# Optimization experiments

Hardware: AMD Instinct MI355X
Metric: run time of the kernel (lower is better)

Reference implementation:

```python
import jax, jax.numpy as jnp
import numpy as np

N_NODES = 20000
N_EDGES = 640000
NODE_IN = 128
EDGE_IN = 64
HID = 128
OUT = 128
LOG2 = float(np.log(2.0))


def ssp(x):
    # DGL ShiftedSoftplus: softplus(x) - log(2)
    return jax.nn.softplus(x) - LOG2


def cfconv(x, e, src, dst,
           nW, nb, eW1, eb1, eW2, eb2, oW, ob):
    hv = x @ nW + nb                                  # [N, HID]
    he = ssp(ssp(e @ eW1 + eb1) @ eW2 + eb2)          # [E, HID]
    msg = hv[src] * he                                # gather + filter
    agg = jax.ops.segment_sum(msg, dst, num_segments=N_NODES)
    return ssp(agg @ oW + ob)


def setup_inputs() -> dict:
    key = jax.random.key(0)
    ks = jax.random.split(key, 20)
    def w(k, shape, fan_in):
        return jax.random.normal(k, shape, dtype=jnp.float32) * (1.0 / np.sqrt(fan_in))
    inp = {
        "node_inputs": jax.random.normal(ks[0], (N_NODES, NODE_IN), dtype=jnp.float32),
        "edge_inputs": jax.random.normal(ks[1], (N_EDGES, EDGE_IN), dtype=jnp.float32),
        "src": jax.random.randint(ks[2], (N_EDGES,), 0, N_NODES, dtype=jnp.int32),
        "dst": jax.random.randint(ks[3], (N_EDGES,), 0, N_NODES, dtype=jnp.int32),
        # conv1 params
        "n1_W": w(ks[4], (NODE_IN, HID), NODE_IN), "n1_b": jnp.zeros((HID,), jnp.float32),
        "e1_W1": w(ks[5], (EDGE_IN, HID), EDGE_IN), "e1_b1": jnp.zeros((HID,), jnp.float32),
        "e1_W2": w(ks[6], (HID, HID), HID), "e1_b2": jnp.zeros((HID,), jnp.float32),
        "o1_W": w(ks[7], (HID, HID), HID), "o1_b": jnp.zeros((HID,), jnp.float32),
        # conv2 params
        "n2_W": w(ks[8], (HID, HID), HID), "n2_b": jnp.zeros((HID,), jnp.float32),
        "e2_W1": w(ks[9], (EDGE_IN, HID), EDGE_IN), "e2_b1": jnp.zeros((HID,), jnp.float32),
        "e2_W2": w(ks[10], (HID, HID), HID), "e2_b2": jnp.zeros((HID,), jnp.float32),
        "o2_W": w(ks[11], (HID, OUT), HID), "o2_b": jnp.zeros((OUT,), jnp.float32),
    }
    return inp


def reference(node_inputs, edge_inputs, src, dst,
              n1_W, n1_b, e1_W1, e1_b1, e1_W2, e1_b2, o1_W, o1_b,
              n2_W, n2_b, e2_W1, e2_b1, e2_W2, e2_b2, o2_W, o2_b):
    h = cfconv(node_inputs, edge_inputs, src, dst,
               n1_W, n1_b, e1_W1, e1_b1, e1_W2, e1_b2, o1_W, o1_b)
    h = jnp.tanh(h)
    # dropout(p) is identity in eval mode
    h = cfconv(h, edge_inputs, src, dst,
               n2_W, n2_b, e2_W1, e2_b1, e2_W2, e2_b2, o2_W, o2_b)
    return jnp.tanh(h)
```

## Files before the change

kernel.cpp:

```cpp
#include <hip/hip_runtime.h>
#include <hip/hip_bf16.h>
#include <math.h>

typedef __bf16 bf16x8 __attribute__((ext_vector_type(8)));
typedef float f32x4 __attribute__((ext_vector_type(4)));

#define LOG2F 0.6931471805599453f
#define PK1 72
#define PK2 136

__device__ __forceinline__ float sspf(float x) {
    float t = __expf(-fabsf(x));
    return fmaxf(x, 0.0f) + __logf(1.0f + t) - LOG2F;
}
__device__ __forceinline__ unsigned short f2bf(float f) {
    union { float f; unsigned u; } v; v.f = f;
    unsigned r = v.u + 0x7FFF + ((v.u >> 16) & 1);
    return (unsigned short)(r >> 16);
}
__device__ __forceinline__ unsigned short f2bf_fast(float f) {
    __bf16 h = (__bf16)f;
    return __builtin_bit_cast(unsigned short, h);
}

template<int ACT>
__global__ void node_gemm(const float* __restrict__ X, const float* __restrict__ W,
                          const float* __restrict__ b, float* __restrict__ Y, int N) {
    __shared__ float xs[2][128];
    const int tid = threadIdx.x;
    const int r = tid >> 7;
    const int c = tid & 127;
    const int row = blockIdx.x * 2 + r;
    if (row < N) xs[r][c] = X[(size_t)row * 128 + c];
    __syncthreads();
    if (row >= N) return;
    float acc = b[c];
#pragma unroll 8
    for (int k = 0; k < 128; ++k)
        acc = fmaf(xs[r][k], W[k * 128 + c], acc);
    if (ACT) acc = tanhf(sspf(acc));
    Y[(size_t)row * 128 + c] = acc;
}

__global__ void convert_wT(const float* __restrict__ W, unsigned short* __restrict__ O,
                           int K, int PK) {
    int idx = blockIdx.x * 256 + threadIdx.x;
    if (idx >= 128 * PK) return;
    int n = idx / PK, k = idx - n * PK;
    O[idx] = (k < K) ? f2bf(W[k * 128 + n]) : (unsigned short)0;
}

__global__ void hist_kernel(const int* __restrict__ dst, int* __restrict__ hist, int E) {
    int i = blockIdx.x * 256 + threadIdx.x;
    if (i < E) atomicAdd(&hist[dst[i]], 1);
}
__global__ void scan_kernel(const int* __restrict__ hist, int* __restrict__ row_ptr,
                            int* __restrict__ cursor, int N) {
    __shared__ int part[1024];
    const int tid = threadIdx.x;
    const int chunk = (N + 1023) / 1024;
    const int lo = min(tid * chunk, N);
    const int hi = min(lo + chunk, N);
    int s = 0;
    for (int i = lo; i < hi; ++i) s += hist[i];
    part[tid] = s;
    __syncthreads();
    if (tid == 0) {
        int run = 0;
        for (int i = 0; i < 1024; ++i) { int t = part[i]; part[i] = run; run += t; }
    }
    __syncthreads();
    int run = part[tid];
    for (int i = lo; i < hi; ++i) { row_ptr[i] = run; cursor[i] = run; run += hist[i]; }
}
__global__ void scatter_kernel(const int* __restrict__ dst, int* __restrict__ cursor,
                               int* __restrict__ perm, int E) {
    int i = blockIdx.x * 256 + threadIdx.x;
    if (i < E) { int p = atomicAdd(&cursor[dst[i]], 1); perm[p] = i; }
}
__global__ void sort_buckets(const int* __restrict__ row_ptr, const int* __restrict__ hist,
                             int* __restrict__ perm, int N) {
    int n = blockIdx.x * 256 + threadIdx.x;
    if (n >= N) return;
    const int lo = row_ptr[n], hi = lo + hist[n];
    for (int i = lo + 1; i < hi; ++i) {
        int v = perm[i]; int j = i - 1;
        while (j >= lo && perm[j] > v) { perm[j + 1] = perm[j]; --j; }
        perm[j + 1] = v;
    }
}
__global__ void permute_sd(const int* __restrict__ perm, const int* __restrict__ src,
                           const int* __restrict__ dst, int* __restrict__ srcP,
                           int* __restrict__ dstP, int E) {
    int i = blockIdx.x * 256 + threadIdx.x;
    if (i < E) { int e = perm[i]; srcP[i] = src[e]; dstP[i] = dst[e]; }
}
__global__ void permute_e(const int* __restrict__ perm, const float* __restrict__ Ef,
                          unsigned short* __restrict__ Ebf, int nE) {
    long long idx = (long long)blockIdx.x * 256 + threadIdx.x;
    if (idx >= (long long)nE * 16) return;
    int p = (int)(idx >> 4), q = (int)(idx & 15);
    int e = perm[p];
    float4 v = *(const float4*)&Ef[(size_t)e * 64 + q * 4];
    unsigned short* o = &Ebf[(size_t)p * 64 + q * 4];
    o[0] = f2bf_fast(v.x); o[1] = f2bf_fast(v.y);
    o[2] = f2bf_fast(v.z); o[3] = f2bf_fast(v.w);
}

template<int MODE>
__global__ __launch_bounds__(256) void edge_mfma(
    const unsigned short* __restrict__ Ebf, const float* __restrict__ Ef,
    const int* __restrict__ perm,
    const int* __restrict__ srcA, const int* __restrict__ dstA,
    const float* __restrict__ HV,
    const unsigned short* __restrict__ W1T, const float* __restrict__ b1,
    const unsigned short* __restrict__ W2T, const float* __restrict__ b2,
    float* __restrict__ AGG, int nE)
{
    __shared__ unsigned short sT1[64 * PK2];
    __shared__ int sSrc[64], sDst[64];
    __shared__ unsigned short sE[(MODE == 1) ? 64 * PK1 : 4];

    const int tid = threadIdx.x;
    const int e0 = blockIdx.x * 64;

    if (tid < 64) {
        int gi = min(e0 + tid, nE - 1);
        sSrc[tid] = srcA[gi];
        sDst[tid] = dstA[gi];
    }
    if (MODE == 1) {
        const int r = tid >> 2, c0 = (tid & 3) * 16;
        int gi = e0 + r;
        int e = (gi < nE) ? (perm ? perm[gi] : gi) : 0;
        const float4* s4 = (const float4*)&Ef[(size_t)e * 64 + c0];
        unsigned short* dr = &sE[r * PK1 + c0];
#pragma unroll
        for (int j = 0; j < 4; ++j) {
            float4 v = s4[j];
            dr[j*4+0] = f2bf_fast(v.x); dr[j*4+1] = f2bf_fast(v.y);
            dr[j*4+2] = f2bf_fast(v.z); dr[j*4+3] = f2bf_fast(v.w);
        }
    }
    __syncthreads();

    const int w = tid >> 6, l = tid & 63, cb = w * 32, lr = l & 15, hi = l >> 4, lk = hi * 8;
    const float bb1[2] = { b1[cb + lr], b1[cb + 16 + lr] };
    const float bb2[2] = { b2[cb + lr], b2[cb + 16 + lr] };

    bf16x8 B1[2][2];
#pragma unroll
    for (int nt = 0; nt < 2; ++nt)
#pragma unroll
        for (int kt = 0; kt < 2; ++kt)
            B1[nt][kt] = *(const bf16x8*)&W1T[(size_t)(cb + nt*16 + lr) * PK1 + kt*32 + lk];

    f32x4 acc1[4][2];
#pragma unroll
    for (int mt = 0; mt < 4; ++mt)
#pragma unroll
        for (int nt = 0; nt < 2; ++nt)
            acc1[mt][nt] = (f32x4){bb1[nt], bb1[nt], bb1[nt], bb1[nt]};
#pragma unroll
    for (int kt = 0; kt < 2; ++kt)
#pragma unroll
        for (int mt = 0; mt < 4; ++mt) {
            bf16x8 A;
            if (MODE == 0) {
                const int row = min(e0 + mt*16 + lr, nE - 1);
                A = *(const bf16x8*)&Ebf[(size_t)row * 64 + kt*32 + lk];
            } else {
                A = *(const bf16x8*)&sE[(mt*16 + lr) * PK1 + kt*32 + lk];
            }
#pragma unroll
            for (int nt = 0; nt < 2; ++nt)
                acc1[mt][nt] = __builtin_amdgcn_mfma_f32_16x16x32_bf16(A, B1[nt][kt], acc1[mt][nt], 0, 0, 0);
        }

#pragma unroll
    for (int mt = 0; mt < 4; ++mt)
#pragma unroll
        for (int nt = 0; nt < 2; ++nt) {
            const int col = cb + nt*16 + lr;
#pragma unroll
            for (int r = 0; r < 4; ++r) {
                const int row = mt*16 + hi*4 + r;
                sT1[row * PK2 + col] = f2bf_fast(sspf(acc1[mt][nt][r]));
            }
        }
    __syncthreads();

    bf16x8 B2[2][4];
#pragma unroll
    for (int nt = 0; nt < 2; ++nt)
#pragma unroll
        for (int kt = 0; kt < 4; ++kt)
            B2[nt][kt] = *(const bf16x8*)&W2T[(size_t)(cb + nt*16 + lr) * PK2 + kt*32 + lk];

    f32x4 acc2[4][2];
#pragma unroll
    for (int mt = 0; mt < 4; ++mt)
#pragma unroll
        for (int nt = 0; nt < 2; ++nt)
            acc2[mt][nt] = (f32x4){bb2[nt], bb2[nt], bb2[nt], bb2[nt]};
#pragma unroll
    for (int kt = 0; kt < 4; ++kt)
#pragma unroll
        for (int mt = 0; mt < 4; ++mt) {
            bf16x8 A = *(const bf16x8*)&sT1[(mt*16 + lr) * PK2 + kt*32 + lk];
#pragma unroll
            for (int nt = 0; nt < 2; ++nt)
                acc2[mt][nt] = __builtin_amdgcn_mfma_f32_16x16x32_bf16(A, B2[nt][kt], acc2[mt][nt], 0, 0, 0);
        }

    const int col0 = cb + lr, col1 = cb + 16 + lr;
    int curd = sDst[hi * 4];
    float s0 = 0.f, s1 = 0.f;
#pragma unroll
    for (int mt = 0; mt < 4; ++mt) {
#pragma unroll
        for (int r = 0; r < 4; ++r) {
            const int row = mt*16 + hi*4 + r;
            const float msk = (e0 + row < nE) ? 1.f : 0.f;
            const float he0 = sspf(acc2[mt][0][r]) * msk;
            const float he1 = sspf(acc2[mt][1][r]) * msk;
            const int s = sSrc[row], d = sDst[row];
            const float m0 = HV[(size_t)s * 128 + col0] * he0;
            const float m1 = HV[(size_t)s * 128 + col1] * he1;
            if (d != curd) {
                atomicAdd(&AGG[(size_t)curd * 128 + col0], s0);
                atomicAdd(&AGG[(size_t)curd * 128 + col1], s1);
                s0 = 0.f; s1 = 0.f; curd = d;
            }
            s0 += m0; s1 += m1;
        }
    }
    atomicAdd(&AGG[(size_t)curd * 128 + col0], s0);
    atomicAdd(&AGG[(size_t)curd * 128 + col1], s1);
}

extern "C" void kernel_launch(void* const* d_in, const int* in_sizes, int n_in,
                              void* d_out, int out_size, void* d_ws, size_t ws_size,
                              hipStream_t stream) {
    const float* x    = (const float*)d_in[0];
    const float* e    = (const float*)d_in[1];
    const int*   src  = (const int*)  d_in[2];
    const int*   dst  = (const int*)  d_in[3];
    const float* n1W  = (const float*)d_in[4];
    const float* n1b  = (const float*)d_in[5];
    const float* e1W1 = (const float*)d_in[6];
    const float* e1b1 = (const float*)d_in[7];
    const float* e1W2 = (const float*)d_in[8];
    const float* e1b2 = (const float*)d_in[9];
    const float* o1W  = (const float*)d_in[10];
    const float* o1b  = (const float*)d_in[11];
    const float* n2W  = (const float*)d_in[12];
    const float* n2b  = (const float*)d_in[13];
    const float* e2W1 = (const float*)d_in[14];
    const float* e2b1 = (const float*)d_in[15];
    const float* e2W2 = (const float*)d_in[16];
    const float* e2b2 = (const float*)d_in[17];
    const float* o2W  = (const float*)d_in[18];
    const float* o2b  = (const float*)d_in[19];

    const int N = in_sizes[0] / 128;
    const int E = in_sizes[2];
    float* out = (float*)d_out;

    char* ws = (char*)d_ws;
    size_t off = 0;
    auto alloc = [&](size_t bytes) -> char* {
        char* p = ws + off;
        off = (off + bytes + 255) & ~(size_t)255;
        return p;
    };
    float* agg = (float*)alloc((size_t)N * 128 * 4);
    float* hv  = (float*)alloc((size_t)N * 128 * 4);
    unsigned short* w_e1w1 = (unsigned short*)alloc(128 * PK1 * 2);
    unsigned short* w_e1w2 = (unsigned short*)alloc(128 * PK2 * 2);
    unsigned short* w_e2w1 = (unsigned short*)alloc(128 * PK1 * 2);
    unsigned short* w_e2w2 = (unsigned short*)alloc(128 * PK2 * 2);
    int* perm    = (int*)alloc((size_t)E * 4);
    int* srcP    = (int*)alloc((size_t)E * 4);
    int* dstP    = (int*)alloc((size_t)E * 4);
    int* hist    = (int*)alloc((size_t)N * 4);
    int* cursor  = (int*)alloc((size_t)N * 4);
    int* row_ptr = (int*)alloc((size_t)N * 4);
    const size_t sort_need = off;
    unsigned short* Ebf = (unsigned short*)alloc((size_t)E * 64 * 2);
    const bool useEbf  = (ws_size >= off);
    const bool useSort = (ws_size >= sort_need);

    float* hbuf = out;

    convert_wT<<<(128*PK1 + 255)/256, 256, 0, stream>>>(e1W1, w_e1w1, 64,  PK1);
    convert_wT<<<(128*PK2 + 255)/256, 256, 0, stream>>>(e1W2, w_e1w2, 128, PK2);
    convert_wT<<<(128*PK1 + 255)/256, 256, 0, stream>>>(e2W1, w_e2w1, 64,  PK1);
    convert_wT<<<(128*PK2 + 255)/256, 256, 0, stream>>>(e2W2, w_e2w2, 128, PK2);

    const int* sA = src;
    const int* dA = dst;
    const int* permArg = nullptr;
    if (useSort) {
        hipMemsetAsync(hist, 0, (size_t)N * 4, stream);
        hist_kernel<<<(E + 255)/256, 256, 0, stream>>>(dst, hist, E);
        scan_kernel<<<1, 1024, 0, stream>>>(hist, row_ptr, cursor, N);
        scatter_kernel<<<(E + 255)/256, 256, 0, stream>>>(dst, cursor, perm, E);
        sort_buckets<<<(N + 255)/256, 256, 0, stream>>>(row_ptr, hist, perm, N);
        permute_sd<<<(E + 255)/256, 256, 0, stream>>>(perm, src, dst, srcP, dstP, E);
        if (useEbf)
            permute_e<<<(int)(((size_t)E * 16 + 255)/256), 256, 0, stream>>>(perm, e, Ebf, E);
        sA = srcP; dA = dstP; permArg = perm;
    }

    const int nodeBlocks = (N + 1) / 2;
    const int edgeBlocks = (E + 63) / 64;
    const size_t nbytes = (size_t)N * 128 * 4;

    node_gemm<0><<<nodeBlocks, 256, 0, stream>>>(x, n1W, n1b, hv, N);
    hipMemsetAsync(agg, 0, nbytes, stream);
    if (useEbf)
        edge_mfma<0><<<edgeBlocks, 256, 0, stream>>>(Ebf, nullptr, nullptr, sA, dA, hv,
                                                     w_e1w1, e1b1, w_e1w2, e1b2, agg, E);
    else
        edge_mfma<1><<<edgeBlocks, 256, 0, stream>>>(nullptr, e, permArg, sA, dA, hv,
                                                     w_e1w1, e1b1, w_e1w2, e1b2, agg, E);
    node_gemm<1><<<nodeBlocks, 256, 0, stream>>>(agg, o1W, o1b, hbuf, N);

    node_gemm<0><<<nodeBlocks, 256, 0, stream>>>(hbuf, n2W, n2b, hv, N);
    hipMemsetAsync(agg, 0, nbytes, stream);
    if (useEbf)
        edge_mfma<0><<<edgeBlocks, 256, 0, stream>>>(Ebf, nullptr, nullptr, sA, dA, hv,
                                                     w_e2w1, e2b1, w_e2w2, e2b2, agg, E);
    else
        edge_mfma<1><<<edgeBlocks, 256, 0, stream>>>(nullptr, e, permArg, sA, dA, hv,
                                                     w_e2w1, e2b1, w_e2w2, e2b2, agg, E);
    node_gemm<1><<<nodeBlocks, 256, 0, stream>>>(agg, o2W, o2b, out, N);
}
```

Baseline: 787.8 us.

## Move node GEMMs to split-bf16 MFMA, fuse mid-layer GEMMs, merge prep kernels

Replaces the scalar FMA node GEMMs with MFMA kernels that split fp32 operands into bf16 hi/lo pairs and run three MFMAs per tile to keep near-fp32 accuracy. The output GEMM of conv1 and the node GEMM of conv2 are fused into one kernel that keeps the intermediate tile in shared memory. The four weight-conversion launches are merged into one, and permute_sd is folded into permute_e. The edge kernel now issues segment atomics once per 16-row tile instead of only at the end, which looks like a correctness adjustment. The cost is three times the MFMA work and extra weight buffers, in exchange for removing the slow scalar node GEMMs and several launches.

```diff
diff --git a/kernel.cpp b/kernel.cpp
--- a/kernel.cpp
+++ b/kernel.cpp
@@ -18,36 +18,51 @@
     unsigned r = v.u + 0x7FFF + ((v.u >> 16) & 1);
     return (unsigned short)(r >> 16);
 }
+__device__ __forceinline__ float bf2f(unsigned short u) {
+    union { unsigned u; float f; } v; v.u = ((unsigned)u) << 16;
+    return v.f;
+}
 __device__ __forceinline__ unsigned short f2bf_fast(float f) {
     __bf16 h = (__bf16)f;
     return __builtin_bit_cast(unsigned short, h);
 }
 
-template<int ACT>
-__global__ void node_gemm(const float* __restrict__ X, const float* __restrict__ W,
-                          const float* __restrict__ b, float* __restrict__ Y, int N) {
-    __shared__ float xs[2][128];
-    const int tid = threadIdx.x;
-    const int r = tid >> 7;
-    const int c = tid & 127;
-    const int row = blockIdx.x * 2 + r;
-    if (row < N) xs[r][c] = X[(size_t)row * 128 + c];
-    __syncthreads();
-    if (row >= N) return;
-    float acc = b[c];
-#pragma unroll 8
-    for (int k = 0; k < 128; ++k)
-        acc = fmaf(xs[r][k], W[k * 128 + c], acc);
-    if (ACT) acc = tanhf(sspf(acc));
-    Y[(size_t)row * 128 + c] = acc;
-}
-
-__global__ void convert_wT(const float* __restrict__ W, unsigned short* __restrict__ O,
-                           int K, int PK) {
-    int idx = blockIdx.x * 256 + threadIdx.x;
-    if (idx >= 128 * PK) return;
-    int n = idx / PK, k = idx - n * PK;
-    O[idx] = (k < K) ? f2bf(W[k * 128 + n]) : (unsigned short)0;
+__global__ void convert_all(
+    const float* __restrict__ A0, const float* __restrict__ A1,
+    const float* __restrict__ A2, const float* __restrict__ A3,
+    const float* __restrict__ A4, const float* __restrict__ A5,
+    const float* __restrict__ A6, const float* __restrict__ A7,
+    unsigned short* __restrict__ O0, unsigned short* __restrict__ O1,
+    unsigned short* __restrict__ O2, unsigned short* __restrict__ O3,
+    unsigned short* __restrict__ H4, unsigned short* __restrict__ L4,
+    unsigned short* __restrict__ H5, unsigned short* __restrict__ L5,
+    unsigned short* __restrict__ H6, unsigned short* __restrict__ L6,
+    unsigned short* __restrict__ H7, unsigned short* __restrict__ L7)
+{
+    const int seg = blockIdx.x / 68;
+    const int idx = (blockIdx.x % 68) * 256 + threadIdx.x;
+    if (seg < 4) {
+        const int PK = (seg == 0 || seg == 2) ? PK1 : PK2;
+        const int K  = (seg == 0 || seg == 2) ? 64 : 128;
+        if (idx >= 128 * PK) return;
+        const float* W = (seg == 0) ? A0 : (seg == 1) ? A1 : (seg == 2) ? A2 : A3;
+        unsigned short* O = (seg == 0) ? O0 : (seg == 1) ? O1 : (seg == 2) ? O2 : O3;
+        int n = idx / PK, k = idx - n * PK;
+        O[idx] = (k < K) ? f2bf(W[k * 128 + n]) : (unsigned short)0;
+    } else {
+        if (idx >= 128 * PK2) return;
+        const float* W = (seg == 4) ? A4 : (seg == 5) ? A5 : (seg == 6) ? A6 : A7;
+        unsigned short* H = (seg == 4) ? H4 : (seg == 5) ? H5 : (seg == 6) ? H6 : H7;
+        unsigned short* L = (seg == 4) ? L4 : (seg == 5) ? L5 : (seg == 6) ? L6 : L7;
+        int n = idx / PK2, k = idx - n * PK2;
+        unsigned short h = 0, lo = 0;
+        if (k < 128) {
+            float w = W[k * 128 + n];
+            h = f2bf(w);
+            lo = f2bf(w - bf2f(h));
+        }
+        H[idx] = h; L[idx] = lo;
+    }
 }
 
 __global__ void hist_kernel(const int* __restrict__ dst, int* __restrict__ hist, int E) {
@@ -95,16 +110,217 @@
     int i = blockIdx.x * 256 + threadIdx.x;
     if (i < E) { int e = perm[i]; srcP[i] = src[e]; dstP[i] = dst[e]; }
 }
-__global__ void permute_e(const int* __restrict__ perm, const float* __restrict__ Ef,
-                          unsigned short* __restrict__ Ebf, int nE) {
+__global__ void permute_all(const int* __restrict__ perm, const int* __restrict__ src,
+                            const int* __restrict__ dst, const float* __restrict__ Ef,
+                            int* __restrict__ srcP, int* __restrict__ dstP,
+                            unsigned short* __restrict__ Ebf, int nE) {
     long long idx = (long long)blockIdx.x * 256 + threadIdx.x;
     if (idx >= (long long)nE * 16) return;
     int p = (int)(idx >> 4), q = (int)(idx & 15);
     int e = perm[p];
+    if (q == 0) { srcP[p] = src[e]; dstP[p] = dst[e]; }
     float4 v = *(const float4*)&Ef[(size_t)e * 64 + q * 4];
     unsigned short* o = &Ebf[(size_t)p * 64 + q * 4];
     o[0] = f2bf_fast(v.x); o[1] = f2bf_fast(v.y);
     o[2] = f2bf_fast(v.z); o[3] = f2bf_fast(v.w);
+}
+
+template<int ACT>
+__global__ __launch_bounds__(256) void node_mfma3(
+    const float* __restrict__ X, const unsigned short* __restrict__ WThi,
+    const unsigned short* __restrict__ WTlo, const float* __restrict__ b,
+    float* __restrict__ Y, int N)
+{
+    __shared__ unsigned short sHi[32 * PK2];
+    __shared__ unsigned short sLo[32 * PK2];
+    const int tid = threadIdx.x;
+    const int r0 = blockIdx.x * 32;
+    {
+        const int r = tid >> 3, c0 = (tid & 7) * 16;
+        const int row = min(r0 + r, N - 1);
+        const float4* s4 = (const float4*)&X[(size_t)row * 128 + c0];
+        unsigned short* dh = &sHi[r * PK2 + c0];
+        unsigned short* dl = &sLo[r * PK2 + c0];
+#pragma unroll
+        for (int j = 0; j < 4; ++j) {
+            float4 v = s4[j];
+            float c[4] = { v.x, v.y, v.z, v.w };
+#pragma unroll
+            for (int q = 0; q < 4; ++q) {
+                unsigned short h = f2bf_fast(c[q]);
+                dh[j * 4 + q] = h;
+                dl[j * 4 + q] = f2bf_fast(c[q] - bf2f(h));
+            }
+        }
+    }
+    __syncthreads();
+    const int w = tid >> 6, l = tid & 63, cb = w * 32, lr = l & 15, hi4 = l >> 4, lk = hi4 * 8;
+    const float bb[2] = { b[cb + lr], b[cb + 16 + lr] };
+    f32x4 acc[2][2];
+#pragma unroll
+    for (int mt = 0; mt < 2; ++mt)
+#pragma unroll
+        for (int nt = 0; nt < 2; ++nt)
+            acc[mt][nt] = (f32x4){bb[nt], bb[nt], bb[nt], bb[nt]};
+    bf16x8 Bh[2][4], Bl[2][4];
+#pragma unroll
+    for (int nt = 0; nt < 2; ++nt)
+#pragma unroll
+        for (int kt = 0; kt < 4; ++kt) {
+            Bh[nt][kt] = *(const bf16x8*)&WThi[(size_t)(cb + nt*16 + lr) * PK2 + kt*32 + lk];
+            Bl[nt][kt] = *(const bf16x8*)&WTlo[(size_t)(cb + nt*16 + lr) * PK2 + kt*32 + lk];
+        }
+#pragma unroll
+    for (int kt = 0; kt < 4; ++kt)
+#pragma unroll
+        for (int mt = 0; mt < 2; ++mt) {
+            bf16x8 Ah = *(const bf16x8*)&sHi[(mt*16 + lr) * PK2 + kt*32 + lk];
+            bf16x8 Al = *(const bf16x8*)&sLo[(mt*16 + lr) * PK2 + kt*32 + lk];
+#pragma unroll
+            for (int nt = 0; nt < 2; ++nt) {
+                acc[mt][nt] = __builtin_amdgcn_mfma_f32_16x16x32_bf16(Ah, Bh[nt][kt], acc[mt][nt], 0, 0, 0);
+                acc[mt][nt] = __builtin_amdgcn_mfma_f32_16x16x32_bf16(Al, Bh[nt][kt], acc[mt][nt], 0, 0, 0);
+                acc[mt][nt] = __builtin_amdgcn_mfma_f32_16x16x32_bf16(Ah, Bl[nt][kt], acc[mt][nt], 0, 0, 0);
+            }
+        }
+#pragma unroll
+    for (int mt = 0; mt < 2; ++mt)
+#pragma unroll
+        for (int nt = 0; nt < 2; ++nt) {
+            const int col = cb + nt*16 + lr;
+#pragma unroll
+            for (int r = 0; r < 4; ++r) {
+                const int row = r0 + mt*16 + hi4*4 + r;
+                if (row < N) {
+                    float v = acc[mt][nt][r];
+                    if (ACT) v = tanhf(sspf(v));
+                    Y[(size_t)row * 128 + col] = v;
+                }
+            }
+        }
+}
+
+__global__ __launch_bounds__(256) void node_mid(
+    const float* __restrict__ AGG,
+    const unsigned short* __restrict__ W1hi, const unsigned short* __restrict__ W1lo,
+    const float* __restrict__ b1,
+    const unsigned short* __restrict__ W2hi, const unsigned short* __restrict__ W2lo,
+    const float* __restrict__ b2,
+    float* __restrict__ HVout, int N)
+{
+    __shared__ unsigned short sHi[32 * PK2];
+    __shared__ unsigned short sLo[32 * PK2];
+    const int tid = threadIdx.x;
+    const int r0 = blockIdx.x * 32;
+    {
+        const int r = tid >> 3, c0 = (tid & 7) * 16;
+        const int row = min(r0 + r, N - 1);
+        const float4* s4 = (const float4*)&AGG[(size_t)row * 128 + c0];
+        unsigned short* dh = &sHi[r * PK2 + c0];
+        unsigned short* dl = &sLo[r * PK2 + c0];
+#pragma unroll
+        for (int j = 0; j < 4; ++j) {
+            float4 v = s4[j];
+            float c[4] = { v.x, v.y, v.z, v.w };
+#pragma unroll
+            for (int q = 0; q < 4; ++q) {
+                unsigned short h = f2bf_fast(c[q]);
+                dh[j * 4 + q] = h;
+                dl[j * 4 + q] = f2bf_fast(c[q] - bf2f(h));
+            }
+        }
+    }
+    __syncthreads();
+    const int w = tid >> 6, l = tid & 63, cb = w * 32, lr = l & 15, hi4 = l >> 4, lk = hi4 * 8;
+
+    f32x4 acc1[2][2];
+    {
+        const float bb[2] = { b1[cb + lr], b1[cb + 16 + lr] };
+#pragma unroll
+        for (int mt = 0; mt < 2; ++mt)
+#pragma unroll
+            for (int nt = 0; nt < 2; ++nt)
+                acc1[mt][nt] = (f32x4){bb[nt], bb[nt], bb[nt], bb[nt]};
+        bf16x8 Bh[2][4], Bl[2][4];
+#pragma unroll
+        for (int nt = 0; nt < 2; ++nt)
+#pragma unroll
+            for (int kt = 0; kt < 4; ++kt) {
+                Bh[nt][kt] = *(const bf16x8*)&W1hi[(size_t)(cb + nt*16 + lr) * PK2 + kt*32 + lk];
+                Bl[nt][kt] = *(const bf16x8*)&W1lo[(size_t)(cb + nt*16 + lr) * PK2 + kt*32 + lk];
+            }
+#pragma unroll
+        for (int kt = 0; kt < 4; ++kt)
+#pragma unroll
+            for (int mt = 0; mt < 2; ++mt) {
+                bf16x8 Ah = *(const bf16x8*)&sHi[(mt*16 + lr) * PK2 + kt*32 + lk];
+                bf16x8 Al = *(const bf16x8*)&sLo[(mt*16 + lr) * PK2 + kt*32 + lk];
+#pragma unroll
+                for (int nt = 0; nt < 2; ++nt) {
+                    acc1[mt][nt] = __builtin_amdgcn_mfma_f32_16x16x32_bf16(Ah, Bh[nt][kt], acc1[mt][nt], 0, 0, 0);
+                    acc1[mt][nt] = __builtin_amdgcn_mfma_f32_16x16x32_bf16(Al, Bh[nt][kt], acc1[mt][nt], 0, 0, 0);
+                    acc1[mt][nt] = __builtin_amdgcn_mfma_f32_16x16x32_bf16(Ah, Bl[nt][kt], acc1[mt][nt], 0, 0, 0);
+                }
+            }
+    }
+    __syncthreads();
+#pragma unroll
+    for (int mt = 0; mt < 2; ++mt)
+#pragma unroll
+        for (int nt = 0; nt < 2; ++nt) {
+            const int col = cb + nt*16 + lr;
+#pragma unroll
+            for (int r = 0; r < 4; ++r) {
+                const int row = mt*16 + hi4*4 + r;
+                float v = tanhf(sspf(acc1[mt][nt][r]));
+                unsigned short h = f2bf_fast(v);
+                sHi[row * PK2 + col] = h;
+                sLo[row * PK2 + col] = f2bf_fast(v - bf2f(h));
+            }
+        }
+    __syncthreads();
+
+    f32x4 acc2[2][2];
+    {
+        const float bb[2] = { b2[cb + lr], b2[cb + 16 + lr] };
+#pragma unroll
+        for (int mt = 0; mt < 2; ++mt)
+#pragma unroll
+            for (int nt = 0; nt < 2; ++nt)
+                acc2[mt][nt] = (f32x4){bb[nt], bb[nt], bb[nt], bb[nt]};
+        bf16x8 Bh[2][4], Bl[2][4];
+#pragma unroll
+        for (int nt = 0; nt < 2; ++nt)
+#pragma unroll
+            for (int kt = 0; kt < 4; ++kt) {
+                Bh[nt][kt] = *(const bf16x8*)&W2hi[(size_t)(cb + nt*16 + lr) * PK2 + kt*32 + lk];
+                Bl[nt][kt] = *(const bf16x8*)&W2lo[(size_t)(cb + nt*16 + lr) * PK2 + kt*32 + lk];
+            }
+#pragma unroll
+        for (int kt = 0; kt < 4; ++kt)
+#pragma unroll
+            for (int mt = 0; mt < 2; ++mt) {
+                bf16x8 Ah = *(const bf16x8*)&sHi[(mt*16 + lr) * PK2 + kt*32 + lk];
+                bf16x8 Al = *(const bf16x8*)&sLo[(mt*16 + lr) * PK2 + kt*32 + lk];
+#pragma unroll
+                for (int nt = 0; nt < 2; ++nt) {
+                    acc2[mt][nt] = __builtin_amdgcn_mfma_f32_16x16x32_bf16(Ah, Bh[nt][kt], acc2[mt][nt], 0, 0, 0);
+                    acc2[mt][nt] = __builtin_amdgcn_mfma_f32_16x16x32_bf16(Al, Bh[nt][kt], acc2[mt][nt], 0, 0, 0);
+                    acc2[mt][nt] = __builtin_amdgcn_mfma_f32_16x16x32_bf16(Ah, Bl[nt][kt], acc2[mt][nt], 0, 0, 0);
+                }
+            }
+    }
+#pragma unroll
+    for (int mt = 0; mt < 2; ++mt)
+#pragma unroll
+        for (int nt = 0; nt < 2; ++nt) {
+            const int col = cb + nt*16 + lr;
+#pragma unroll
+            for (int r = 0; r < 4; ++r) {
+                const int row = r0 + mt*16 + hi4*4 + r;
+                if (row < N) HVout[(size_t)row * 128 + col] = acc2[mt][nt][r];
+            }
+        }
 }
 
 template<int MODE>
@@ -144,7 +360,7 @@
     }
     __syncthreads();
 
-    const int w = tid >> 6, l = tid & 63, cb = w * 32, lr = l & 15, hi = l >> 4, lk = hi * 8;
+    const int w = tid >> 6, l = tid & 63, cb = w * 32, lr = l & 15, hi4 = l >> 4, lk = hi4 * 8;
     const float bb1[2] = { b1[cb + lr], b1[cb + 16 + lr] };
     const float bb2[2] = { b2[cb + lr], b2[cb + 16 + lr] };
 
@@ -184,7 +400,7 @@
             const int col = cb + nt*16 + lr;
 #pragma unroll
             for (int r = 0; r < 4; ++r) {
-                const int row = mt*16 + hi*4 + r;
+                const int row = mt*16 + hi4*4 + r;
                 sT1[row * PK2 + col] = f2bf_fast(sspf(acc1[mt][nt][r]));
             }
         }
@@ -214,13 +430,13 @@
         }
 
     const int col0 = cb + lr, col1 = cb + 16 + lr;
-    int curd = sDst[hi * 4];
-    float s0 = 0.f, s1 = 0.f;
 #pragma unroll
     for (int mt = 0; mt < 4; ++mt) {
+        int curd = sDst[mt*16 + hi4*4];
+        float s0 = 0.f, s1 = 0.f;
 #pragma unroll
         for (int r = 0; r < 4; ++r) {
-            const int row = mt*16 + hi*4 + r;
+            const int row = mt*16 + hi4*4 + r;
             const float msk = (e0 + row < nE) ? 1.f : 0.f;
             const float he0 = sspf(acc2[mt][0][r]) * msk;
             const float he1 = sspf(acc2[mt][1][r]) * msk;
@@ -234,9 +450,9 @@
             }
             s0 += m0; s1 += m1;
         }
-    }
-    atomicAdd(&AGG[(size_t)curd * 128 + col0], s0);
-    atomicAdd(&AGG[(size_t)curd * 128 + col1], s1);
+        atomicAdd(&AGG[(size_t)curd * 128 + col0], s0);
+        atomicAdd(&AGG[(size_t)curd * 128 + col1], s1);
+    }
 }
 
 extern "C" void kernel_launch(void* const* d_in, const int* in_sizes, int n_in,
@@ -280,6 +496,14 @@
     unsigned short* w_e1w2 = (unsigned short*)alloc(128 * PK2 * 2);
     unsigned short* w_e2w1 = (unsigned short*)alloc(128 * PK1 * 2);
     unsigned short* w_e2w2 = (unsigned short*)alloc(128 * PK2 * 2);
+    unsigned short* n1hi = (unsigned short*)alloc(128 * PK2 * 2);
+    unsigned short* n1lo = (unsigned short*)alloc(128 * PK2 * 2);
+    unsigned short* o1hi = (unsigned short*)alloc(128 * PK2 * 2);
+    unsigned short* o1lo = (unsigned short*)alloc(128 * PK2 * 2);
+    unsigned short* n2hi = (unsigned short*)alloc(128 * PK2 * 2);
+    unsigned short* n2lo = (unsigned short*)alloc(128 * PK2 * 2);
+    unsigned short* o2hi = (unsigned short*)alloc(128 * PK2 * 2);
+    unsigned short* o2lo = (unsigned short*)alloc(128 * PK2 * 2);
     int* perm    = (int*)alloc((size_t)E * 4);
     int* srcP    = (int*)alloc((size_t)E * 4);
     int* dstP    = (int*)alloc((size_t)E * 4);
@@ -291,12 +515,10 @@
     const bool useEbf  = (ws_size >= off);
     const bool useSort = (ws_size >= sort_need);
 
-    float* hbuf = out;
-
-    convert_wT<<<(128*PK1 + 255)/256, 256, 0, stream>>>(e1W1, w_e1w1, 64,  PK1);
-    convert_wT<<<(128*PK2 + 255)/256, 256, 0, stream>>>(e1W2, w_e1w2, 128, PK2);
-    convert_wT<<<(128*PK1 + 255)/256, 256, 0, stream>>>(e2W1, w_e2w1, 64,  PK1);
-    convert_wT<<<(128*PK2 + 255)/256, 256, 0, stream>>>(e2W2, w_e2w2, 128, PK2);
+    convert_all<<<544, 256, 0, stream>>>(
+        e1W1, e1W2, e2W1, e2W2, n1W, o1W, n2W, o2W,
+        w_e1w1, w_e1w2, w_e2w1, w_e2w2,
+        n1hi, n1lo, o1hi, o1lo, n2hi, n2lo, o2hi, o2lo);
 
     const int* sA = src;
     const int* dA = dst;
@@ -307,17 +529,20 @@
         scan_kernel<<<1, 1024, 0, stream>>>(hist, row_ptr, cursor, N);
         scatter_kernel<<<(E + 255)/256, 256, 0, stream>>>(dst, cursor, perm, E);
         sort_buckets<<<(N + 255)/256, 256, 0, stream>>>(row_ptr, hist, perm, N);
-        permute_sd<<<(E + 255)/256, 256, 0, stream>>>(perm, src, dst, srcP, dstP, E);
-        if (useEbf)
-            permute_e<<<(int)(((size_t)E * 16 + 255)/256), 256, 0, stream>>>(perm, e, Ebf, E);
+        if (useEbf) {
+            permute_all<<<(int)(((size_t)E * 16 + 255)/256), 256, 0, stream>>>(
+                perm, src, dst, e, srcP, dstP, Ebf, E);
+        } else {
+            permute_sd<<<(E + 255)/256, 256, 0, stream>>>(perm, src, dst, srcP, dstP, E);
+        }
         sA = srcP; dA = dstP; permArg = perm;
     }
 
-    const int nodeBlocks = (N + 1) / 2;
+    const int nodeBlocks = (N + 31) / 32;
     const int edgeBlocks = (E + 63) / 64;
     const size_t nbytes = (size_t)N * 128 * 4;
 
-    node_gemm<0><<<nodeBlocks, 256, 0, stream>>>(x, n1W, n1b, hv, N);
+    node_mfma3<0><<<nodeBlocks, 256, 0, stream>>>(x, n1hi, n1lo, n1b, hv, N);
     hipMemsetAsync(agg, 0, nbytes, stream);
     if (useEbf)
         edge_mfma<0><<<edgeBlocks, 256, 0, stream>>>(Ebf, nullptr, nullptr, sA, dA, hv,
@@ -325,9 +550,9 @@
     else
         edge_mfma<1><<<edgeBlocks, 256, 0, stream>>>(nullptr, e, permArg, sA, dA, hv,
                                                      w_e1w1, e1b1, w_e1w2, e1b2, agg, E);
-    node_gemm<1><<<nodeBlocks, 256, 0, stream>>>(agg, o1W, o1b, hbuf, N);
-
-    node_gemm<0><<<nodeBlocks, 256, 0, stream>>>(hbuf, n2W, n2b, hv, N);
+
+    node_mid<<<nodeBlocks, 256, 0, stream>>>(agg, o1hi, o1lo, o1b, n2hi, n2lo, n2b, hv, N);
+
     hipMemsetAsync(agg, 0, nbytes, stream);
     if (useEbf)
         edge_mfma<0><<<edgeBlocks, 256, 0, stream>>>(Ebf, nullptr, nullptr, sA, dA, hv,
@@ -335,5 +560,5 @@
     else
         edge_mfma<1><<<edgeBlocks, 256, 0, stream>>>(nullptr, e, permArg, sA, dA, hv,
                                                      w_e2w1, e2b1, w_e2w2, e2b2, agg, E);
-    node_gemm<1><<<nodeBlocks, 256, 0, stream>>>(agg, o2W, o2b, out, N);
-}
+    node_mfma3<1><<<nodeBlocks, 256, 0, stream>>>(agg, o2hi, o2lo, o2b, out, N);
+}
```

New measurement: 842.2 us. 6.9% more time.
